# Kernel optimization log

Measured on AMD Instinct MI355X. Metric: run time of the kernel, lower is better.

The kernel has to match this reference:

```python
import jax, jax.numpy as jnp
import numpy as np

EPS = 1e-12  # matches torch F.normalize default eps

def setup_inputs() -> dict:
    key = jax.random.key(0)
    k1, k2 = jax.random.split(key)
    query = jax.random.normal(k1, (8, 2048, 512), dtype=jnp.float32)
    support = jax.random.normal(k2, (8, 4096, 512), dtype=jnp.float32)
    return {"query": query, "support": support}

def _l2_normalize(x):
    # torch.nn.functional.normalize(x, dim=-1): x / max(||x||, eps)
    n = jnp.sqrt(jnp.sum(x * x, axis=-1, keepdims=True))
    return x / jnp.maximum(n, EPS)

def reference(query, support):
    # cosine distance: 1 - q_hat @ s_hat^T  -> [B, Nq, Ns]
    qn = _l2_normalize(query)
    sn = _l2_normalize(support)
    dist = 1.0 - jnp.einsum('bqd,bsd->bqs', qn, sn)
    min_d = jnp.min(dist, axis=2)        # [B, Nq]
    return jnp.mean(min_d, axis=1)       # [B]
```

## Files before the change

kernel.cpp:

```cpp
#include <hip/hip_runtime.h>
#include <hip/hip_bf16.h>

typedef __attribute__((ext_vector_type(8))) short short8;
typedef __attribute__((ext_vector_type(4))) float f32x4;
typedef __attribute__((ext_vector_type(16))) float f32x16;
typedef __attribute__((ext_vector_type(8))) int int8v;

#define D   512
#define NQ  2048
#define NS  4096
#define NB  8
#define BM  128
#define BN  128
#define BK  32

typedef const __attribute__((address_space(1))) unsigned int gas_uint;
typedef __attribute__((address_space(3))) unsigned int las_uint;

#define WAIT_VM12  0x0F7C
#define WAIT_VM8   0x0F78
#define WAIT_VM4   0x0F74
#define WAIT_VM0   0x0F70
#define WAIT_LGKM0 0xC07F

__device__ __forceinline__ short f2bf(float f) {
  unsigned u = __builtin_bit_cast(unsigned, f);
  unsigned r = u + 0x7fffu + ((u >> 16) & 1u);
  return (short)(r >> 16);
}

__device__ __forceinline__ short8 pack8(float4 a, float4 b, float r) {
  short8 o;
  o[0] = f2bf(a.x * r); o[1] = f2bf(a.y * r); o[2] = f2bf(a.z * r); o[3] = f2bf(a.w * r);
  o[4] = f2bf(b.x * r); o[5] = f2bf(b.y * r); o[6] = f2bf(b.z * r); o[7] = f2bf(b.w * r);
  return o;
}

__global__ void normcvt8_kernel(const float* __restrict__ q, const float* __restrict__ s,
                                unsigned char* __restrict__ qn, unsigned char* __restrict__ sn,
                                unsigned* __restrict__ maxenc) {
  if (blockIdx.x < 64) maxenc[(blockIdx.x << 8) | threadIdx.x] = 0;
  int wave = blockIdx.x * 4 + (threadIdx.x >> 6);
  int lane = threadIdx.x & 63;
  const int NQR = NB * NQ;
  const float4* src; unsigned char* dst;
  if (wave < NQR) { src = (const float4*)(q + (size_t)wave * D); dst = qn + (size_t)wave * D; }
  else {
    size_t w = wave - NQR;
    src = (const float4*)(s + w * D); dst = sn + w * D;
  }
  float4 a = src[lane * 2];
  float4 b = src[lane * 2 + 1];
  float ss = a.x*a.x + a.y*a.y + a.z*a.z + a.w*a.w
           + b.x*b.x + b.y*b.y + b.z*b.z + b.w*b.w;
  #pragma unroll
  for (int m = 32; m >= 1; m >>= 1) ss += __shfl_xor(ss, m, 64);
  float r = 1.0f / fmaxf(sqrtf(ss), 1e-12f);
  int w0 = __builtin_amdgcn_cvt_pk_fp8_f32(a.x * r, a.y * r, 0, false);
  w0     = __builtin_amdgcn_cvt_pk_fp8_f32(a.z * r, a.w * r, w0, true);
  int w1 = __builtin_amdgcn_cvt_pk_fp8_f32(b.x * r, b.y * r, 0, false);
  w1     = __builtin_amdgcn_cvt_pk_fp8_f32(b.z * r, b.w * r, w1, true);
  *(int2*)(dst + lane * 8) = make_int2(w0, w1);
}

__global__ __launch_bounds__(256, 2) void cosmax15_kernel(
    const unsigned char* __restrict__ Qn, const unsigned char* __restrict__ Sn,
    unsigned int* __restrict__ maxenc)
{
  __shared__ __align__(16) unsigned char sbuf[65536];
  __shared__ float maxbuf[64][4];

  const int id  = blockIdx.x;
  const int b   = id & 7;
  const int j   = id >> 3;
  const int mt  = j & 31;
  const int nsp = j >> 5;
  const int tid  = threadIdx.x;
  const int wave = tid >> 6;
  const int lane = tid & 63;
  const int l31 = lane & 31, kc = lane >> 5;

  {
    const unsigned char* Qbase = Qn + ((size_t)b * NQ + (size_t)mt * 64) * D;
    const int baserow = wave * 2 + (lane >> 5);
    #pragma unroll
    for (int p = 0; p < 8; ++p) {
      int row = p * 8 + baserow;
      int g   = (lane & 31) ^ (row & 31);
      __builtin_amdgcn_global_load_lds(
          (gas_uint*)(Qbase + (size_t)row * D + g * 16),
          (las_uint*)(sbuf + 16384 + p * 4096 + wave * 1024), 16, 0, 0);
    }
  }
  __syncthreads();

  const int srow8 = lane >> 3;
  const int sch   = (lane & 7) ^ srow8;
  const unsigned char* gS = Sn +
      ((size_t)b * NS + (size_t)nsp * 2048 + wave * 32 + srow8) * D + sch * 16;

  auto issue = [&](size_t goff, int ldsoff) {
    #pragma unroll
    for (int t = 0; t < 4; ++t)
      __builtin_amdgcn_global_load_lds((gas_uint*)(gS + goff + (size_t)t * 4096),
          (las_uint*)(sbuf + ldsoff + wave * 4096 + t * 1024), 16, 0, 0);
  };

  issue(0, 0);

  int8v a[2][8];
  #pragma unroll
  for (int m = 0; m < 2; ++m) {
    const int arow = m * 32 + l31;
    #pragma unroll
    for (int kk = 0; kk < 8; ++kk) {
      int c0 = (4 * kk + 2 * kc) ^ l31;
      ((int4*)&a[m][kk])[0] = *(const int4*)&sbuf[16384 + arow * 512 + c0 * 16];
      ((int4*)&a[m][kk])[1] = *(const int4*)&sbuf[16384 + arow * 512 + (c0 ^ 1) * 16];
    }
  }
  __builtin_amdgcn_s_waitcnt(WAIT_LGKM0);
  asm volatile("" ::: "memory");
  __builtin_amdgcn_s_barrier();
  asm volatile("" ::: "memory");
  issue(128, 16384);
  issue(256, 32768);

  const int brow = (wave * 32 + l31) * 128;
  const int cb0  = ((kc * 2) ^ (l31 & 7)) * 16;
  const int cb1  = cb0 ^ 64;

  f32x16 acc0, acc1;
  float rmax0[16], rmax1[16];
  #pragma unroll
  for (int r = 0; r < 16; ++r) { rmax0[r] = -2.0f; rmax1[r] = -2.0f; }

  auto computeK = [&](int kt, int rdo) {
    const unsigned char* Bb = sbuf + rdo;
    int8v b0, b1;
    ((int4*)&b0)[0] = *(const int4*)&Bb[brow + cb0];
    ((int4*)&b0)[1] = *(const int4*)&Bb[brow + (cb0 ^ 16)];
    ((int4*)&b1)[0] = *(const int4*)&Bb[brow + cb1];
    ((int4*)&b1)[1] = *(const int4*)&Bb[brow + (cb1 ^ 16)];
    __builtin_amdgcn_s_setprio(1);
    acc0 = __builtin_amdgcn_mfma_scale_f32_32x32x64_f8f6f4(
        a[0][kt * 2], b0, acc0, 0, 0, 0, 0x7f7f7f7f, 0, 0x7f7f7f7f);
    acc1 = __builtin_amdgcn_mfma_scale_f32_32x32x64_f8f6f4(
        a[1][kt * 2], b0, acc1, 0, 0, 0, 0x7f7f7f7f, 0, 0x7f7f7f7f);
    acc0 = __builtin_amdgcn_mfma_scale_f32_32x32x64_f8f6f4(
        a[0][kt * 2 + 1], b1, acc0, 0, 0, 0, 0x7f7f7f7f, 0, 0x7f7f7f7f);
    acc1 = __builtin_amdgcn_mfma_scale_f32_32x32x64_f8f6f4(
        a[1][kt * 2 + 1], b1, acc1, 0, 0, 0, 0x7f7f7f7f, 0, 0x7f7f7f7f);
    __builtin_amdgcn_s_setprio(0);
  };

  #define KSTEP(WAITIMM)                       \
    asm volatile("" ::: "memory");             \
    __builtin_amdgcn_s_waitcnt(WAITIMM);       \
    asm volatile("" ::: "memory");

  #pragma clang loop unroll(disable)
  for (int nt2 = 0; nt2 < 16; ++nt2) {
    const size_t ntb = (size_t)nt2 << 16;
    const bool more = (nt2 < 15);

    #pragma unroll
    for (int r = 0; r < 16; ++r) { acc0[r] = 0.f; acc1[r] = 0.f; }

    issue(ntb + 384, 49152);
    KSTEP(WAIT_VM12);
    computeK(0, 0);

    if (more) { issue(ntb + 65536, 0); KSTEP(WAIT_VM12); }
    else      { KSTEP(WAIT_VM8); }
    computeK(1, 16384);

    if (more) { issue(ntb + 65536 + 128, 16384); KSTEP(WAIT_VM12); }
    else      { KSTEP(WAIT_VM4); }
    computeK(2, 32768);

    if (more) { issue(ntb + 65536 + 256, 32768); KSTEP(WAIT_VM12); }
    else      { KSTEP(WAIT_VM0); }
    computeK(3, 49152);

    #pragma unroll
    for (int r = 0; r < 16; ++r) {
      rmax0[r] = fmaxf(rmax0[r], acc0[r]);
      rmax1[r] = fmaxf(rmax1[r], acc1[r]);
    }
  }
  #undef KSTEP

  #pragma unroll
  for (int m = 0; m < 2; ++m) {
    #pragma unroll
    for (int r = 0; r < 16; ++r) {
      float v = m ? rmax1[r] : rmax0[r];
      v = fmaxf(v, __shfl_xor(v, 1, 64));
      v = fmaxf(v, __shfl_xor(v, 2, 64));
      v = fmaxf(v, __shfl_xor(v, 4, 64));
      v = fmaxf(v, __shfl_xor(v, 8, 64));
      v = fmaxf(v, __shfl_xor(v, 16, 64));
      if (l31 == 0)
        maxbuf[m * 32 + (r & 3) + 8 * (r >> 2) + 4 * kc][wave] = v;
    }
  }
  __syncthreads();

  if (tid < 64) {
    float v = fmaxf(fmaxf(maxbuf[tid][0], maxbuf[tid][1]),
                    fmaxf(maxbuf[tid][2], maxbuf[tid][3]));
    unsigned e = __builtin_bit_cast(unsigned, v);
    e = ((int)e >= 0) ? (e | 0x80000000u) : ~e;
    atomicMax(&maxenc[(size_t)b * NQ + (size_t)mt * 64 + tid], e);
  }
}

__global__ void finalize_kernel(const unsigned* __restrict__ maxenc,
                                float* __restrict__ out) {
  int b = blockIdx.x;
  int tid = threadIdx.x;
  float sum = 0.f;
  for (int i = tid; i < NQ; i += 256) {
    unsigned e = maxenc[(size_t)b * NQ + i];
    unsigned u = (e & 0x80000000u) ? (e & 0x7fffffffu) : ~e;
    float v = __builtin_bit_cast(float, u);
    sum += 1.0f - v;
  }
  #pragma unroll
  for (int m = 32; m >= 1; m >>= 1) sum += __shfl_xor(sum, m, 64);
  __shared__ float part[4];
  if ((tid & 63) == 0) part[tid >> 6] = sum;
  __syncthreads();
  if (tid == 0) out[b] = (part[0] + part[1] + part[2] + part[3]) * (1.0f / (float)NQ);
}

__global__ void norms_kernel(const float* __restrict__ q, const float* __restrict__ s,
                             float* __restrict__ rq, float* __restrict__ rs) {
  int wave = blockIdx.x * 4 + (threadIdx.x >> 6);
  int lane = threadIdx.x & 63;
  const int NQR = NB * NQ, NSR = NB * NS;
  if (wave >= NQR + NSR) return;
  const float4* r4; float* outp;
  if (wave < NQR) { r4 = (const float4*)(q + (size_t)wave * D); outp = rq + wave; }
  else           { r4 = (const float4*)(s + (size_t)(wave - NQR) * D); outp = rs + (wave - NQR); }
  float4 a = r4[lane];
  float4 b = r4[lane + 64];
  float ss = a.x*a.x + a.y*a.y + a.z*a.z + a.w*a.w
           + b.x*b.x + b.y*b.y + b.z*b.z + b.w*b.w;
  #pragma unroll
  for (int m = 32; m >= 1; m >>= 1) ss += __shfl_xor(ss, m, 64);
  if (lane == 0) *outp = 1.0f / fmaxf(sqrtf(ss), 1e-12f);
}

__global__ __launch_bounds__(256, 3) void cosmax_kernel(
    const float* __restrict__ Q, const float* __restrict__ S,
    const float* __restrict__ rq, const float* __restrict__ rs,
    unsigned int* __restrict__ maxenc)
{
  __shared__ short As[BM * BK];
  __shared__ short Bs[BN * BK];
  __shared__ float maxbuf[BM][2];

  const int b  = blockIdx.z, mt = blockIdx.y, nt = blockIdx.x;
  const float* Qb  = Q + ((size_t)b * NQ + mt * BM) * D;
  const float* Sb  = S + ((size_t)b * NS + nt * BN) * D;
  const float* rqb = rq + (size_t)b * NQ + mt * BM;
  const float* rsb = rs + (size_t)b * NS + nt * BN;

  const int tid  = threadIdx.x;
  const int srow = tid >> 2;
  const int kseg = (tid & 3) * 8;
  const float rq0 = rqb[srow], rq1 = rqb[srow + 64];
  const float rs0 = rsb[srow], rs1 = rsb[srow + 64];
  const int wave = tid >> 6, lane = tid & 63;
  const int wm = (wave & 1) * 64, wn = (wave >> 1) * 64;
  const int lm = lane & 15, lk = (lane >> 4) * 8;

  f32x4 acc[4][4];
  #pragma unroll
  for (int i = 0; i < 4; ++i)
    #pragma unroll
    for (int j = 0; j < 4; ++j) acc[i][j] = (f32x4){0.f, 0.f, 0.f, 0.f};

  const float* qrow0 = Qb + (size_t)srow * D + kseg;
  const float* qrow1 = qrow0 + (size_t)64 * D;
  const float* srow0 = Sb + (size_t)srow * D + kseg;
  const float* srow1 = srow0 + (size_t)64 * D;

  float4 qa, qb2, qc, qd, sa, sb2, sc, sd;
  #define LOADK(k0)                                                    \
    qa  = *(const float4*)(qrow0 + (k0));  qb2 = *(const float4*)(qrow0 + (k0) + 4); \
    qc  = *(const float4*)(qrow1 + (k0));  qd  = *(const float4*)(qrow1 + (k0) + 4); \
    sa  = *(const float4*)(srow0 + (k0));  sb2 = *(const float4*)(srow0 + (k0) + 4); \
    sc  = *(const float4*)(srow1 + (k0));  sd  = *(const float4*)(srow1 + (k0) + 4);
  LOADK(0);
  #pragma unroll 4
  for (int kt = 0; kt < D / BK; ++kt) {
    *(short8*)&As[srow        * BK + kseg] = pack8(qa, qb2, rq0);
    *(short8*)&As[(srow + 64) * BK + kseg] = pack8(qc, qd,  rq1);
    *(short8*)&Bs[srow        * BK + kseg] = pack8(sa, sb2, rs0);
    *(short8*)&Bs[(srow + 64) * BK + kseg] = pack8(sc, sd,  rs1);
    __syncthreads();
    if (kt < D / BK - 1) { LOADK((kt + 1) * BK); }
    short8 af[4], bf[4];
    #pragma unroll
    for (int i = 0; i < 4; ++i) af[i] = *(short8*)&As[(wm + i * 16 + lm) * BK + lk];
    #pragma unroll
    for (int j = 0; j < 4; ++j) bf[j] = *(short8*)&Bs[(wn + j * 16 + lm) * BK + lk];
    #pragma unroll
    for (int i = 0; i < 4; ++i)
      #pragma unroll
      for (int j = 0; j < 4; ++j)
        acc[i][j] = __builtin_amdgcn_mfma_f32_16x16x32_bf16(af[i], bf[j], acc[i][j], 0, 0, 0);
    __syncthreads();
  }
  #undef LOADK

  #pragma unroll
  for (int i = 0; i < 4; ++i) {
    #pragma unroll
    for (int r = 0; r < 4; ++r) {
      float v = fmaxf(fmaxf(acc[i][0][r], acc[i][1][r]),
                      fmaxf(acc[i][2][r], acc[i][3][r]));
      v = fmaxf(v, __shfl_xor(v, 1, 64));
      v = fmaxf(v, __shfl_xor(v, 2, 64));
      v = fmaxf(v, __shfl_xor(v, 4, 64));
      v = fmaxf(v, __shfl_xor(v, 8, 64));
      if ((lane & 15) == 0) {
        int row = wm + i * 16 + (lane >> 4) * 4 + r;
        maxbuf[row][wave >> 1] = v;
      }
    }
  }
  __syncthreads();
  if (tid < BM) {
    float v = fmaxf(maxbuf[tid][0], maxbuf[tid][1]);
    unsigned e = __builtin_bit_cast(unsigned, v);
    e = ((int)e >= 0) ? (e | 0x80000000u) : ~e;
    atomicMax(&maxenc[(size_t)b * NQ + mt * BM + tid], e);
  }
}

extern "C" void kernel_launch(void* const* d_in, const int* in_sizes, int n_in,
                              void* d_out, int out_size, void* d_ws, size_t ws_size,
                              hipStream_t stream) {
  const float* q = (const float*)d_in[0];
  const float* s = (const float*)d_in[1];
  float* out = (float*)d_out;

  unsigned* maxenc = (unsigned*)d_ws;
  const size_t QOFF = 65536;
  const size_t SOFF = QOFF + (size_t)NB * NQ * D;
  const size_t NEED = SOFF + (size_t)NB * NS * D;

  if (ws_size >= NEED) {
    unsigned char* qn = (unsigned char*)d_ws + QOFF;
    unsigned char* sn = (unsigned char*)d_ws + SOFF;
    normcvt8_kernel<<<NB * (NQ + NS) / 4, 256, 0, stream>>>(q, s, qn, sn, maxenc);
    cosmax15_kernel<<<512, 256, 0, stream>>>(qn, sn, maxenc);
    finalize_kernel<<<NB, 256, 0, stream>>>(maxenc, out);
  } else {
    float* rq = (float*)((char*)d_ws + 65536);
    float* rs = (float*)((char*)d_ws + 131072);
    hipMemsetAsync(maxenc, 0, (size_t)NB * NQ * sizeof(unsigned), stream);
    norms_kernel<<<NB * (NQ + NS) / 4, 256, 0, stream>>>(q, s, rq, rs);
    dim3 grid(NS / BN, NQ / BM, NB);
    cosmax_kernel<<<grid, 256, 0, stream>>>(q, s, rq, rs, maxenc);
    finalize_kernel<<<NB, 256, 0, stream>>>(maxenc, out);
  }
}
```

Before: 160.0 us.

## Fuse normalize, cosine-max GEMM and finalize into one cooperative kernel

Replaces the three-kernel sequence (normalize+fp8 convert, fp8 MFMA cosine-max, mean finalize) with a single cooperative kernel of 512 blocks that uses grid-wide syncs between phases. The aim is to remove the launch gaps and tail idling between the kernels. The cost is two grid barriers, plus the requirement that all 512 blocks are co-resident, which depends on the 64KB+ LDS footprint and two blocks per CU. If the cooperative launch fails, it falls back to the old three-kernel path.

```diff
diff --git a/kernel.cpp b/kernel.cpp
--- a/kernel.cpp
+++ b/kernel.cpp
@@ -1,5 +1,8 @@
 #include <hip/hip_runtime.h>
 #include <hip/hip_bf16.h>
+#include <hip/hip_cooperative_groups.h>
+
+namespace cg = cooperative_groups;
 
 typedef __attribute__((ext_vector_type(8))) short short8;
 typedef __attribute__((ext_vector_type(4))) float f32x4;
@@ -34,6 +37,212 @@
   o[0] = f2bf(a.x * r); o[1] = f2bf(a.y * r); o[2] = f2bf(a.z * r); o[3] = f2bf(a.w * r);
   o[4] = f2bf(b.x * r); o[5] = f2bf(b.y * r); o[6] = f2bf(b.z * r); o[7] = f2bf(b.w * r);
   return o;
+}
+
+__global__ __launch_bounds__(256, 2) void fused17_kernel(
+    const float* __restrict__ q, const float* __restrict__ s,
+    unsigned char* __restrict__ qn, unsigned char* __restrict__ sn,
+    unsigned int* __restrict__ maxenc, float* __restrict__ out)
+{
+  __shared__ __align__(16) unsigned char sbuf[65536];
+  __shared__ float maxbuf[64][4];
+  __shared__ float part[4];
+
+  const int id   = blockIdx.x;
+  const int b    = id & 7;
+  const int g    = id >> 3;
+  const int tid  = threadIdx.x;
+  const int wave = tid >> 6;
+  const int lane = tid & 63;
+
+  if (id < 64) maxenc[(id << 8) | tid] = 0;
+  #pragma clang loop unroll(disable)
+  for (int k = 0; k < 24; ++k) {
+    const int rib = (g * 4 + wave) + (k << 8);
+    const float4* src; unsigned char* dst;
+    if (rib < 2048) {
+      src = (const float4*)(q + ((size_t)b * NQ + rib) * D);
+      dst = qn + ((size_t)b * NQ + rib) * D;
+    } else {
+      const int r2 = rib - 2048;
+      src = (const float4*)(s + ((size_t)b * NS + r2) * D);
+      dst = sn + ((size_t)b * NS + r2) * D;
+    }
+    float4 va = src[lane * 2];
+    float4 vb = src[lane * 2 + 1];
+    float ss = va.x*va.x + va.y*va.y + va.z*va.z + va.w*va.w
+             + vb.x*vb.x + vb.y*vb.y + vb.z*vb.z + vb.w*vb.w;
+    #pragma unroll
+    for (int m = 32; m >= 1; m >>= 1) ss += __shfl_xor(ss, m, 64);
+    float r = 1.0f / fmaxf(sqrtf(ss), 1e-12f);
+    int w0 = __builtin_amdgcn_cvt_pk_fp8_f32(va.x * r, va.y * r, 0, false);
+    w0     = __builtin_amdgcn_cvt_pk_fp8_f32(va.z * r, va.w * r, w0, true);
+    int w1 = __builtin_amdgcn_cvt_pk_fp8_f32(vb.x * r, vb.y * r, 0, false);
+    w1     = __builtin_amdgcn_cvt_pk_fp8_f32(vb.z * r, vb.w * r, w1, true);
+    *(int2*)(dst + lane * 8) = make_int2(w0, w1);
+  }
+
+  cg::this_grid().sync();
+
+  {
+    const int j   = id >> 3;
+    const int mt  = j & 31;
+    const int nsp = j >> 5;
+    const int l31 = lane & 31, kc = lane >> 5;
+
+    {
+      const unsigned char* Qbase = qn + ((size_t)b * NQ + (size_t)mt * 64) * D;
+      const int baserow = wave * 2 + (lane >> 5);
+      #pragma unroll
+      for (int p = 0; p < 8; ++p) {
+        int row = p * 8 + baserow;
+        int gsw = (lane & 31) ^ (row & 31);
+        __builtin_amdgcn_global_load_lds(
+            (gas_uint*)(Qbase + (size_t)row * D + gsw * 16),
+            (las_uint*)(sbuf + 16384 + p * 4096 + wave * 1024), 16, 0, 0);
+      }
+    }
+    __syncthreads();
+
+    const int srow8 = lane >> 3;
+    const int sch   = (lane & 7) ^ srow8;
+    const unsigned char* gS = sn +
+        ((size_t)b * NS + (size_t)nsp * 2048 + wave * 32 + srow8) * D + sch * 16;
+
+    auto issue = [&](size_t goff, int ldsoff) {
+      #pragma unroll
+      for (int t = 0; t < 4; ++t)
+        __builtin_amdgcn_global_load_lds((gas_uint*)(gS + goff + (size_t)t * 4096),
+            (las_uint*)(sbuf + ldsoff + wave * 4096 + t * 1024), 16, 0, 0);
+    };
+
+    issue(0, 0);
+
+    int8v a[2][8];
+    #pragma unroll
+    for (int m = 0; m < 2; ++m) {
+      const int arow = m * 32 + l31;
+      #pragma unroll
+      for (int kk = 0; kk < 8; ++kk) {
+        int c0 = (4 * kk + 2 * kc) ^ l31;
+        ((int4*)&a[m][kk])[0] = *(const int4*)&sbuf[16384 + arow * 512 + c0 * 16];
+        ((int4*)&a[m][kk])[1] = *(const int4*)&sbuf[16384 + arow * 512 + (c0 ^ 1) * 16];
+      }
+    }
+    __builtin_amdgcn_s_waitcnt(WAIT_LGKM0);
+    asm volatile("" ::: "memory");
+    __builtin_amdgcn_s_barrier();
+    asm volatile("" ::: "memory");
+    issue(128, 16384);
+    issue(256, 32768);
+
+    const int brow = (wave * 32 + l31) * 128;
+    const int cb0  = ((kc * 2) ^ (l31 & 7)) * 16;
+    const int cb1  = cb0 ^ 64;
+
+    f32x16 acc0, acc1;
+    float rmax0[16], rmax1[16];
+    #pragma unroll
+    for (int r = 0; r < 16; ++r) { rmax0[r] = -2.0f; rmax1[r] = -2.0f; }
+
+    auto computeK = [&](int kt, int rdo) {
+      const unsigned char* Bb = sbuf + rdo;
+      int8v b0, b1;
+      ((int4*)&b0)[0] = *(const int4*)&Bb[brow + cb0];
+      ((int4*)&b0)[1] = *(const int4*)&Bb[brow + (cb0 ^ 16)];
+      ((int4*)&b1)[0] = *(const int4*)&Bb[brow + cb1];
+      ((int4*)&b1)[1] = *(const int4*)&Bb[brow + (cb1 ^ 16)];
+      __builtin_amdgcn_s_setprio(1);
+      acc0 = __builtin_amdgcn_mfma_scale_f32_32x32x64_f8f6f4(
+          a[0][kt * 2], b0, acc0, 0, 0, 0, 0x7f7f7f7f, 0, 0x7f7f7f7f);
+      acc1 = __builtin_amdgcn_mfma_scale_f32_32x32x64_f8f6f4(
+          a[1][kt * 2], b0, acc1, 0, 0, 0, 0x7f7f7f7f, 0, 0x7f7f7f7f);
+      acc0 = __builtin_amdgcn_mfma_scale_f32_32x32x64_f8f6f4(
+          a[0][kt * 2 + 1], b1, acc0, 0, 0, 0, 0x7f7f7f7f, 0, 0x7f7f7f7f);
+      acc1 = __builtin_amdgcn_mfma_scale_f32_32x32x64_f8f6f4(
+          a[1][kt * 2 + 1], b1, acc1, 0, 0, 0, 0x7f7f7f7f, 0, 0x7f7f7f7f);
+      __builtin_amdgcn_s_setprio(0);
+    };
+
+    #define KSTEP(WAITIMM)                       \
+      asm volatile("" ::: "memory");             \
+      __builtin_amdgcn_s_waitcnt(WAITIMM);       \
+      asm volatile("" ::: "memory");
+
+    #pragma clang loop unroll(disable)
+    for (int nt2 = 0; nt2 < 16; ++nt2) {
+      const size_t ntb = (size_t)nt2 << 16;
+      const bool more = (nt2 < 15);
+
+      #pragma unroll
+      for (int r = 0; r < 16; ++r) { acc0[r] = 0.f; acc1[r] = 0.f; }
+
+      issue(ntb + 384, 49152);
+      KSTEP(WAIT_VM12);
+      computeK(0, 0);
+
+      if (more) { issue(ntb + 65536, 0); KSTEP(WAIT_VM12); }
+      else      { KSTEP(WAIT_VM8); }
+      computeK(1, 16384);
+
+      if (more) { issue(ntb + 65536 + 128, 16384); KSTEP(WAIT_VM12); }
+      else      { KSTEP(WAIT_VM4); }
+      computeK(2, 32768);
+
+      if (more) { issue(ntb + 65536 + 256, 32768); KSTEP(WAIT_VM12); }
+      else      { KSTEP(WAIT_VM0); }
+      computeK(3, 49152);
+
+      #pragma unroll
+      for (int r = 0; r < 16; ++r) {
+        rmax0[r] = fmaxf(rmax0[r], acc0[r]);
+        rmax1[r] = fmaxf(rmax1[r], acc1[r]);
+      }
+    }
+    #undef KSTEP
+
+    #pragma unroll
+    for (int m = 0; m < 2; ++m) {
+      #pragma unroll
+      for (int r = 0; r < 16; ++r) {
+        float v = m ? rmax1[r] : rmax0[r];
+        v = fmaxf(v, __shfl_xor(v, 1, 64));
+        v = fmaxf(v, __shfl_xor(v, 2, 64));
+        v = fmaxf(v, __shfl_xor(v, 4, 64));
+        v = fmaxf(v, __shfl_xor(v, 8, 64));
+        v = fmaxf(v, __shfl_xor(v, 16, 64));
+        if (l31 == 0)
+          maxbuf[m * 32 + (r & 3) + 8 * (r >> 2) + 4 * kc][wave] = v;
+      }
+    }
+    __syncthreads();
+
+    if (tid < 64) {
+      float v = fmaxf(fmaxf(maxbuf[tid][0], maxbuf[tid][1]),
+                      fmaxf(maxbuf[tid][2], maxbuf[tid][3]));
+      unsigned e = __builtin_bit_cast(unsigned, v);
+      e = ((int)e >= 0) ? (e | 0x80000000u) : ~e;
+      atomicMax(&maxenc[(size_t)b * NQ + (size_t)mt * 64 + tid], e);
+    }
+  }
+
+  cg::this_grid().sync();
+
+  if (id < 8) {
+    float sum = 0.f;
+    for (int i = tid; i < NQ; i += 256) {
+      unsigned e = maxenc[(size_t)id * NQ + i];
+      unsigned u = (e & 0x80000000u) ? (e & 0x7fffffffu) : ~e;
+      float v = __builtin_bit_cast(float, u);
+      sum += 1.0f - v;
+    }
+    #pragma unroll
+    for (int m = 32; m >= 1; m >>= 1) sum += __shfl_xor(sum, m, 64);
+    if ((tid & 63) == 0) part[tid >> 6] = sum;
+    __syncthreads();
+    if (tid == 0)
+      out[id] = (part[0] + part[1] + part[2] + part[3]) * (1.0f / (float)NQ);
+  }
 }
 
 __global__ void normcvt8_kernel(const float* __restrict__ q, const float* __restrict__ s,
@@ -357,9 +566,16 @@
   if (ws_size >= NEED) {
     unsigned char* qn = (unsigned char*)d_ws + QOFF;
     unsigned char* sn = (unsigned char*)d_ws + SOFF;
-    normcvt8_kernel<<<NB * (NQ + NS) / 4, 256, 0, stream>>>(q, s, qn, sn, maxenc);
-    cosmax15_kernel<<<512, 256, 0, stream>>>(qn, sn, maxenc);
-    finalize_kernel<<<NB, 256, 0, stream>>>(maxenc, out);
+
+    void* args[] = { (void*)&q, (void*)&s, (void*)&qn, (void*)&sn,
+                     (void*)&maxenc, (void*)&out };
+    hipError_t err = hipLaunchCooperativeKernel(
+        (const void*)fused17_kernel, dim3(512), dim3(256), args, 0, stream);
+    if (err != hipSuccess) {
+      normcvt8_kernel<<<NB * (NQ + NS) / 4, 256, 0, stream>>>(q, s, qn, sn, maxenc);
+      cosmax15_kernel<<<512, 256, 0, stream>>>(qn, sn, maxenc);
+      finalize_kernel<<<NB, 256, 0, stream>>>(maxenc, out);
+    }
   } else {
     float* rq = (float*)((char*)d_ws + 65536);
     float* rs = (float*)((char*)d_ws + 131072);
```

Measured after the change: 270.5 us. +69.0%, slower.

## Load support tiles directly from global into registers, bypassing LDS staging

Applied to the files above, without the earlier changes.

Each wave's support operand rows are no longer staged in LDS through async global_load_lds with manual waitcnt pipelining. They are now loaded straight from global memory into MFMA B registers, double-buffered one step ahead of compute. The LDS allocation shrinks to the query tile only. This removes LDS round-trips and explicit wait management, but each global load must now be hidden by a single compute step, so it relies on the compiler's waitcnt placement and on cache hits.

```diff
diff --git a/kernel.cpp b/kernel.cpp
--- a/kernel.cpp
+++ b/kernel.cpp
@@ -16,12 +16,6 @@
 
 typedef const __attribute__((address_space(1))) unsigned int gas_uint;
 typedef __attribute__((address_space(3))) unsigned int las_uint;
-
-#define WAIT_VM12  0x0F7C
-#define WAIT_VM8   0x0F78
-#define WAIT_VM4   0x0F74
-#define WAIT_VM0   0x0F70
-#define WAIT_LGKM0 0xC07F
 
 __device__ __forceinline__ short f2bf(float f) {
   unsigned u = __builtin_bit_cast(unsigned, f);
@@ -63,11 +57,11 @@
   *(int2*)(dst + lane * 8) = make_int2(w0, w1);
 }
 
-__global__ __launch_bounds__(256, 2) void cosmax15_kernel(
+__global__ __launch_bounds__(256, 2) void cosmax18_kernel(
     const unsigned char* __restrict__ Qn, const unsigned char* __restrict__ Sn,
     unsigned int* __restrict__ maxenc)
 {
-  __shared__ __align__(16) unsigned char sbuf[65536];
+  __shared__ __align__(16) unsigned char sbuf[32768];
   __shared__ float maxbuf[64][4];
 
   const int id  = blockIdx.x;
@@ -89,24 +83,10 @@
       int g   = (lane & 31) ^ (row & 31);
       __builtin_amdgcn_global_load_lds(
           (gas_uint*)(Qbase + (size_t)row * D + g * 16),
-          (las_uint*)(sbuf + 16384 + p * 4096 + wave * 1024), 16, 0, 0);
+          (las_uint*)(sbuf + p * 4096 + wave * 1024), 16, 0, 0);
     }
   }
   __syncthreads();
-
-  const int srow8 = lane >> 3;
-  const int sch   = (lane & 7) ^ srow8;
-  const unsigned char* gS = Sn +
-      ((size_t)b * NS + (size_t)nsp * 2048 + wave * 32 + srow8) * D + sch * 16;
-
-  auto issue = [&](size_t goff, int ldsoff) {
-    #pragma unroll
-    for (int t = 0; t < 4; ++t)
-      __builtin_amdgcn_global_load_lds((gas_uint*)(gS + goff + (size_t)t * 4096),
-          (las_uint*)(sbuf + ldsoff + wave * 4096 + t * 1024), 16, 0, 0);
-  };
-
-  issue(0, 0);
 
   int8v a[2][8];
   #pragma unroll
@@ -115,73 +95,56 @@
     #pragma unroll
     for (int kk = 0; kk < 8; ++kk) {
       int c0 = (4 * kk + 2 * kc) ^ l31;
-      ((int4*)&a[m][kk])[0] = *(const int4*)&sbuf[16384 + arow * 512 + c0 * 16];
-      ((int4*)&a[m][kk])[1] = *(const int4*)&sbuf[16384 + arow * 512 + (c0 ^ 1) * 16];
-    }
-  }
-  __builtin_amdgcn_s_waitcnt(WAIT_LGKM0);
-  asm volatile("" ::: "memory");
-  __builtin_amdgcn_s_barrier();
-  asm volatile("" ::: "memory");
-  issue(128, 16384);
-  issue(256, 32768);
-
-  const int brow = (wave * 32 + l31) * 128;
-  const int cb0  = ((kc * 2) ^ (l31 & 7)) * 16;
-  const int cb1  = cb0 ^ 64;
+      ((int4*)&a[m][kk])[0] = *(const int4*)&sbuf[arow * 512 + c0 * 16];
+      ((int4*)&a[m][kk])[1] = *(const int4*)&sbuf[arow * 512 + (c0 ^ 1) * 16];
+    }
+  }
+
+  const unsigned char* gB = Sn +
+      ((size_t)b * NS + (size_t)nsp * 2048 + wave * 32 + l31) * D + kc * 32;
+
+  auto LOADB = [&](int8v& b0, int8v& b1, int s) {
+    const unsigned char* p = gB + ((size_t)(s >> 2) << 16) + ((s & 3) << 7);
+    ((int4*)&b0)[0] = *(const int4*)(p);
+    ((int4*)&b0)[1] = *(const int4*)(p + 16);
+    ((int4*)&b1)[0] = *(const int4*)(p + 64);
+    ((int4*)&b1)[1] = *(const int4*)(p + 80);
+  };
 
   f32x16 acc0, acc1;
   float rmax0[16], rmax1[16];
   #pragma unroll
   for (int r = 0; r < 16; ++r) { rmax0[r] = -2.0f; rmax1[r] = -2.0f; }
 
-  auto computeK = [&](int kt, int rdo) {
-    const unsigned char* Bb = sbuf + rdo;
-    int8v b0, b1;
-    ((int4*)&b0)[0] = *(const int4*)&Bb[brow + cb0];
-    ((int4*)&b0)[1] = *(const int4*)&Bb[brow + (cb0 ^ 16)];
-    ((int4*)&b1)[0] = *(const int4*)&Bb[brow + cb1];
-    ((int4*)&b1)[1] = *(const int4*)&Bb[brow + (cb1 ^ 16)];
+  int8v bA0, bA1, bB0, bB1;
+  LOADB(bA0, bA1, 0);
+  LOADB(bB0, bB1, 1);
+
+  auto computeK = [&](int kk2, const int8v& b0, const int8v& b1) {
     __builtin_amdgcn_s_setprio(1);
     acc0 = __builtin_amdgcn_mfma_scale_f32_32x32x64_f8f6f4(
-        a[0][kt * 2], b0, acc0, 0, 0, 0, 0x7f7f7f7f, 0, 0x7f7f7f7f);
+        a[0][kk2], b0, acc0, 0, 0, 0, 0x7f7f7f7f, 0, 0x7f7f7f7f);
     acc1 = __builtin_amdgcn_mfma_scale_f32_32x32x64_f8f6f4(
-        a[1][kt * 2], b0, acc1, 0, 0, 0, 0x7f7f7f7f, 0, 0x7f7f7f7f);
+        a[1][kk2], b0, acc1, 0, 0, 0, 0x7f7f7f7f, 0, 0x7f7f7f7f);
     acc0 = __builtin_amdgcn_mfma_scale_f32_32x32x64_f8f6f4(
-        a[0][kt * 2 + 1], b1, acc0, 0, 0, 0, 0x7f7f7f7f, 0, 0x7f7f7f7f);
+        a[0][kk2 + 1], b1, acc0, 0, 0, 0, 0x7f7f7f7f, 0, 0x7f7f7f7f);
     acc1 = __builtin_amdgcn_mfma_scale_f32_32x32x64_f8f6f4(
-        a[1][kt * 2 + 1], b1, acc1, 0, 0, 0, 0x7f7f7f7f, 0, 0x7f7f7f7f);
+        a[1][kk2 + 1], b1, acc1, 0, 0, 0, 0x7f7f7f7f, 0, 0x7f7f7f7f);
     __builtin_amdgcn_s_setprio(0);
   };
 
-  #define KSTEP(WAITIMM)                       \
-    asm volatile("" ::: "memory");             \
-    __builtin_amdgcn_s_waitcnt(WAITIMM);       \
-    asm volatile("" ::: "memory");
-
   #pragma clang loop unroll(disable)
   for (int nt2 = 0; nt2 < 16; ++nt2) {
-    const size_t ntb = (size_t)nt2 << 16;
+    const int s = nt2 * 4;
     const bool more = (nt2 < 15);
 
     #pragma unroll
     for (int r = 0; r < 16; ++r) { acc0[r] = 0.f; acc1[r] = 0.f; }
 
-    issue(ntb + 384, 49152);
-    KSTEP(WAIT_VM12);
-    computeK(0, 0);
-
-    if (more) { issue(ntb + 65536, 0); KSTEP(WAIT_VM12); }
-    else      { KSTEP(WAIT_VM8); }
-    computeK(1, 16384);
-
-    if (more) { issue(ntb + 65536 + 128, 16384); KSTEP(WAIT_VM12); }
-    else      { KSTEP(WAIT_VM4); }
-    computeK(2, 32768);
-
-    if (more) { issue(ntb + 65536 + 256, 32768); KSTEP(WAIT_VM12); }
-    else      { KSTEP(WAIT_VM0); }
-    computeK(3, 49152);
+    computeK(0, bA0, bA1); LOADB(bA0, bA1, s + 2);
+    computeK(2, bB0, bB1); LOADB(bB0, bB1, s + 3);
+    computeK(4, bA0, bA1); if (more) LOADB(bA0, bA1, s + 4);
+    computeK(6, bB0, bB1); if (more) LOADB(bB0, bB1, s + 5);
 
     #pragma unroll
     for (int r = 0; r < 16; ++r) {
@@ -189,7 +152,6 @@
       rmax1[r] = fmaxf(rmax1[r], acc1[r]);
     }
   }
-  #undef KSTEP
 
   #pragma unroll
   for (int m = 0; m < 2; ++m) {
@@ -358,7 +320,7 @@
     unsigned char* qn = (unsigned char*)d_ws + QOFF;
     unsigned char* sn = (unsigned char*)d_ws + SOFF;
     normcvt8_kernel<<<NB * (NQ + NS) / 4, 256, 0, stream>>>(q, s, qn, sn, maxenc);
-    cosmax15_kernel<<<512, 256, 0, stream>>>(qn, sn, maxenc);
+    cosmax18_kernel<<<512, 256, 0, stream>>>(qn, sn, maxenc);
     finalize_kernel<<<NB, 256, 0, stream>>>(maxenc, out);
   } else {
     float* rq = (float*)((char*)d_ws + 65536);
```

Result: slower. 231.4 us (+44.6%).
